# Kernel tuning notes

Measured on AMD Instinct MI355X. Metric: run time of the kernel, lower is better.

Reference implementation:

```python
import jax, jax.numpy as jnp
import numpy as np

EMB = 2048; H = 32; G = 8; D = 64; GS = H // G; EPS = 1e-6

def _rmsnorm(x, scale):
    x32 = x.astype(jnp.float32)
    var = jnp.mean(x32 * x32, axis=-1, keepdims=True)
    return (x32 * jax.lax.rsqrt(var + EPS) * scale).astype(x.dtype)

def _rope(x, cos, sin):
    # x: [B, h, S, D]; cos/sin: [S, D]
    d = x.shape[-1]
    x1, x2 = x[..., : d // 2], x[..., d // 2 :]
    rot = jnp.concatenate([-x2, x1], axis=-1)
    return (x * cos[None, None] + rot * sin[None, None]).astype(x.dtype)

def setup_inputs() -> dict:
    key = jax.random.key(0)
    ks = jax.random.split(key, 6)
    B, S = 2, 2048
    x = jax.random.normal(ks[0], (B, S, EMB), jnp.float32)
    # causal mask: True = blocked (masked_fill semantics)
    mask = jnp.triu(jnp.ones((S, S), dtype=bool), k=1)
    # standard RoPE tables, half-dim rotation, shape [S, D]
    inv_freq = 1.0 / (10000.0 ** (jnp.arange(0, D, 2, dtype=jnp.float32) / D))
    ang = jnp.arange(S, dtype=jnp.float32)[:, None] * inv_freq[None, :]  # [S, D/2]
    cos = jnp.concatenate([jnp.cos(ang), jnp.cos(ang)], axis=-1)
    sin = jnp.concatenate([jnp.sin(ang), jnp.sin(ang)], axis=-1)
    Wq = jax.random.normal(ks[1], (EMB, H * D), jnp.float32) * 0.02
    Wk = jax.random.normal(ks[2], (EMB, G * D), jnp.float32) * 0.02
    Wv = jax.random.normal(ks[3], (EMB, G * D), jnp.float32) * 0.02
    Wo = jax.random.normal(ks[4], (H * D, EMB), jnp.float32) * 0.02
    q_scale = jnp.ones((D,), jnp.float32)
    k_scale = jnp.ones((D,), jnp.float32)
    return {"x": x, "mask": mask, "cos": cos, "sin": sin, "Wq": Wq, "Wk": Wk,
            "Wv": Wv, "Wo": Wo, "q_scale": q_scale, "k_scale": k_scale}

def reference(x, mask, cos, sin, Wq, Wk, Wv, Wo, q_scale, k_scale):
    B, S, _ = x.shape
    q = (x @ Wq).reshape(B, S, H, D).transpose(0, 2, 1, 3)  # [B,H,S,D]
    k = (x @ Wk).reshape(B, S, G, D).transpose(0, 2, 1, 3)  # [B,G,S,D]
    v = (x @ Wv).reshape(B, S, G, D).transpose(0, 2, 1, 3)
    q = _rmsnorm(q, q_scale)
    k = _rmsnorm(k, k_scale)
    q = _rope(q, cos, sin)
    k = _rope(k, cos, sin)
    # GQA expansion (repeat_interleave over head dim)
    k = jnp.repeat(k, GS, axis=1)
    v = jnp.repeat(v, GS, axis=1)
    scale = 1.0 / np.float32(np.sqrt(D))
    s = jnp.einsum('bhqd,bhkd->bhqk', q.astype(jnp.float32), k.astype(jnp.float32)) * scale
    # flash path is causal regardless of `mask` arg; mask here equals causal
    s = jnp.where(mask[None, None], -jnp.inf, s)
    w = jax.nn.softmax(s, axis=-1)
    ctx = jnp.einsum('bhqk,bhkd->bhqd', w, v.astype(jnp.float32))
    ctx = ctx.transpose(0, 2, 1, 3).reshape(B, S, H * D)
    return ctx @ Wo
```

## Files before the change

### kernel.cpp

```cpp
#include <hip/hip_runtime.h>
#include <hip/hip_bf16.h>
#include <cstdint>
#include <cstddef>

#define EMB   2048
#define NH_   32
#define NG_   8
#define DH_   64
#define SEQ_  2048
#define BB_   2
#define MTOT  4096
#define LDQKV 3072

typedef __attribute__((ext_vector_type(8))) short s16x8;
typedef __attribute__((ext_vector_type(8))) unsigned short u16x8;
typedef __attribute__((ext_vector_type(4))) float f32x4;
typedef __attribute__((ext_vector_type(16))) float f32x16;
typedef __attribute__((ext_vector_type(4))) unsigned int u32x4;
typedef __attribute__((ext_vector_type(2))) unsigned int u32x2;
typedef __attribute__((ext_vector_type(2))) int i32x2;

__device__ __forceinline__ float bf2f(unsigned short u) {
  unsigned int x = (unsigned int)u << 16; return __uint_as_float(x);
}
__device__ __forceinline__ unsigned short f2bf(float f) {
  unsigned int x = __float_as_uint(f);
  x = x + 0x7FFFu + ((x >> 16) & 1u);
  return (unsigned short)(x >> 16);
}
__device__ __forceinline__ float ninf() { return __int_as_float(0xff800000); }
__device__ __forceinline__ unsigned int pack_bf2(float a, float b) {
  unsigned int r;
  asm("v_cvt_pk_bf16_f32 %0, %1, %2" : "=v"(r) : "v"(a), "v"(b));
  return r;
}
__device__ __forceinline__ void plswap(unsigned int& a, unsigned int& b) {
  i32x2 r = __builtin_amdgcn_permlane32_swap((int)a, (int)b, false, false);
  a = (unsigned int)r[0]; b = (unsigned int)r[1];
}
__device__ __forceinline__ void plswapf(float& a, float& b) {
  unsigned int ua = __float_as_uint(a), ub = __float_as_uint(b);
  plswap(ua, ub);
  a = __uint_as_float(ua); b = __uint_as_float(ub);
}

__device__ __forceinline__ void glds16(const void* g, void* l) {
  __builtin_amdgcn_global_load_lds((const __attribute__((address_space(1))) void*)g,
                                   (__attribute__((address_space(3))) void*)l, 16, 0, 0);
}

__global__ __launch_bounds__(256)
void cvtx(const float* __restrict__ x, unsigned short* __restrict__ xb) {
  size_t i = (size_t)blockIdx.x * 256 + threadIdx.x;
  float4 a = *(const float4*)(x + i * 8);
  float4 c = *(const float4*)(x + i * 8 + 4);
  u16x8 o;
  o[0] = f2bf(a.x); o[1] = f2bf(a.y); o[2] = f2bf(a.z); o[3] = f2bf(a.w);
  o[4] = f2bf(c.x); o[5] = f2bf(c.y); o[6] = f2bf(c.z); o[7] = f2bf(c.w);
  *(u16x8*)(xb + i * 8) = o;
}

__global__ __launch_bounds__(256)
void wtrans(const float* __restrict__ in, unsigned short* __restrict__ out, int N) {
  __shared__ float tile[64][65];
  const int tid = threadIdx.x;
  const int n0 = blockIdx.x * 64, k0 = blockIdx.y * 64;
  #pragma unroll
  for (int jj = 0; jj < 4; ++jj) {
    int r = (tid >> 4) + jj * 16;
    int c = (tid & 15) * 4;
    float4 v = *(const float4*)(in + (size_t)(k0 + r) * N + n0 + c);
    tile[r][c] = v.x; tile[r][c + 1] = v.y; tile[r][c + 2] = v.z; tile[r][c + 3] = v.w;
  }
  __syncthreads();
  #pragma unroll
  for (int rep = 0; rep < 2; ++rep) {
    int u = rep * 256 + tid;
    int nl = u >> 3, ch = u & 7;
    u16x8 o;
    #pragma unroll
    for (int e = 0; e < 8; ++e) o[e] = f2bf(tile[ch * 8 + e][nl]);
    *(u16x8*)(out + (size_t)(n0 + nl) * 2048 + k0 + ch * 8) = o;
  }
}

__global__ __launch_bounds__(512, 2)
void gemm256(const unsigned short* __restrict__ A, const unsigned short* __restrict__ Bt,
             unsigned short* __restrict__ C, int ldc) {
  __shared__ __align__(16) char L[4][32768];
  const int tid = threadIdx.x;
  const int wid = tid >> 6, lane = tid & 63;
  const int wm = wid >> 2, wn = wid & 3;
  const int grp = lane >> 4, l15 = lane & 15;
  const int bm = blockIdx.y * 256, bn = blockIdx.x * 256;
  const int nt = 2048 / 32;

  const int srow = tid >> 2;
  const int sc = (tid & 3) ^ (srow & 3);
  const int grp2 = grp ^ (l15 & 3);

  auto stage_ht = [&](int t, int h) {
    const unsigned short* src = (h < 2)
      ? A  + (size_t)(bm + h * 128 + srow) * 2048 + t * 32 + sc * 8
      : Bt + (size_t)(bn + (h - 2) * 128 + srow) * 2048 + t * 32 + sc * 8;
    glds16(src, &L[t & 3][h * 8192 + wid * 1024]);
  };

  f32x4 acc[8][4] = {};

  #pragma unroll
  for (int h = 0; h < 4; ++h) stage_ht(0, h);
  #pragma unroll
  for (int h = 0; h < 4; ++h) stage_ht(1, h);
  asm volatile("s_waitcnt vmcnt(4)" ::: "memory");
  __builtin_amdgcn_sched_barrier(0);
  __builtin_amdgcn_s_barrier();
  __builtin_amdgcn_sched_barrier(0);

  for (int t = 0; t < nt; ++t) {
    const char* Ab = &L[t & 3][0]     + (size_t)(wm * 128 + l15) * 64 + grp2 * 16;
    const char* Bb = &L[t & 3][16384] + (size_t)(wn * 64  + l15) * 64 + grp2 * 16;
    const bool pre = (t + 2 < nt);
    if (pre) { stage_ht(t + 2, 0); stage_ht(t + 2, 1); }
    s16x8 bf[4], af[4];
    #pragma unroll
    for (int j = 0; j < 4; ++j) bf[j] = *(const s16x8*)(Bb + j * 1024);
    #pragma unroll
    for (int i = 0; i < 4; ++i) af[i] = *(const s16x8*)(Ab + i * 1024);
    __builtin_amdgcn_s_setprio(1);
    #pragma unroll
    for (int i = 0; i < 4; ++i)
      #pragma unroll
      for (int j = 0; j < 4; ++j)
        acc[i][j] = __builtin_amdgcn_mfma_f32_16x16x32_bf16(af[i], bf[j], acc[i][j], 0, 0, 0);
    __builtin_amdgcn_s_setprio(0);
    if (pre) { stage_ht(t + 2, 2); stage_ht(t + 2, 3); }
    #pragma unroll
    for (int i = 0; i < 4; ++i) af[i] = *(const s16x8*)(Ab + (4 + i) * 1024);
    __builtin_amdgcn_s_setprio(1);
    #pragma unroll
    for (int i = 0; i < 4; ++i)
      #pragma unroll
      for (int j = 0; j < 4; ++j)
        acc[4 + i][j] = __builtin_amdgcn_mfma_f32_16x16x32_bf16(af[i], bf[j], acc[4 + i][j], 0, 0, 0);
    __builtin_amdgcn_s_setprio(0);
    if (t + 1 < nt) {
      if (pre) asm volatile("s_waitcnt vmcnt(4)" ::: "memory");
      else     asm volatile("s_waitcnt vmcnt(0)" ::: "memory");
      __builtin_amdgcn_sched_barrier(0);
      __builtin_amdgcn_s_barrier();
      __builtin_amdgcn_sched_barrier(0);
    }
  }

  #pragma unroll
  for (int i = 0; i < 8; ++i)
    #pragma unroll
    for (int j = 0; j < 4; ++j)
      #pragma unroll
      for (int r = 0; r < 4; ++r) {
        int row = bm + wm * 128 + i * 16 + grp * 4 + r;
        int col = bn + wn * 64 + j * 16 + l15;
        C[(size_t)row * ldc + col] = f2bf(acc[i][j][r]);
      }
}

template<int BF16OUT>
__global__ __launch_bounds__(256)
void gemm_bt(const unsigned short* __restrict__ A, const unsigned short* __restrict__ Bt,
             void* __restrict__ C, int ldc) {
  __shared__ __align__(16) unsigned short As[128 * 32];
  __shared__ __align__(16) unsigned short Bs[128 * 32];
  const int tid = threadIdx.x;
  const int w = tid >> 6, lane = tid & 63;
  const int grp = lane >> 4, l15 = lane & 15;
  const int wr = w >> 1, wc = w & 1;
  const int bm = blockIdx.y * 128, bn = blockIdx.x * 128;
  f32x4 acc[4][4] = {};
  for (int k0 = 0; k0 < 2048; k0 += 32) {
    #pragma unroll
    for (int j = 0; j < 2; ++j) {
      int unit = (j * 4 + w) * 64 + lane;
      int row = unit >> 2, ch = unit & 3;
      glds16(A  + (size_t)(bm + row) * 2048 + k0 + ch * 8, (char*)As + (j * 4 + w) * 1024);
      glds16(Bt + (size_t)(bn + row) * 2048 + k0 + ch * 8, (char*)Bs + (j * 4 + w) * 1024);
    }
    __syncthreads();
    s16x8 af[4], bf[4];
    #pragma unroll
    for (int i = 0; i < 4; ++i)
      af[i] = *(const s16x8*)((const char*)As + (wr * 64 + i * 16 + l15) * 64 + grp * 16);
    #pragma unroll
    for (int j = 0; j < 4; ++j)
      bf[j] = *(const s16x8*)((const char*)Bs + (wc * 64 + j * 16 + l15) * 64 + grp * 16);
    #pragma unroll
    for (int i = 0; i < 4; ++i)
      #pragma unroll
      for (int j = 0; j < 4; ++j)
        acc[i][j] = __builtin_amdgcn_mfma_f32_16x16x32_bf16(af[i], bf[j], acc[i][j], 0, 0, 0);
    __syncthreads();
  }
  #pragma unroll
  for (int i = 0; i < 4; ++i)
    #pragma unroll
    for (int j = 0; j < 4; ++j)
      #pragma unroll
      for (int r = 0; r < 4; ++r) {
        int row = bm + wr * 64 + i * 16 + grp * 4 + r;
        int col = bn + wc * 64 + j * 16 + l15;
        float v = acc[i][j][r];
        if (BF16OUT) ((unsigned short*)C)[(size_t)row * ldc + col] = f2bf(v);
        else         ((float*)C)[(size_t)row * ldc + col] = v;
      }
}

__global__ __launch_bounds__(256)
void rmsrope(unsigned short* __restrict__ t, const float* __restrict__ scale,
             const float* __restrict__ cs, const float* __restrict__ sn, int coff, float post) {
  int m = blockIdx.x * 4 + (threadIdx.x >> 6);
  int h = blockIdx.y;
  int lane = threadIdx.x & 63;
  int spos = m & (SEQ_ - 1);
  unsigned short* p = t + (size_t)m * LDQKV + coff + h * 64 + lane;
  float val = bf2f(*p);
  float sq = val * val;
  #pragma unroll
  for (int off = 32; off; off >>= 1) sq += __shfl_xor(sq, off);
  float r = rsqrtf(sq * (1.f / 64.f) + 1e-6f);
  float xn = val * r * scale[lane];
  float partner = __shfl_xor(xn, 32);
  float c = cs[spos * 64 + lane], s = sn[spos * 64 + lane];
  float o = (lane < 32) ? (xn * c - partner * s) : fmaf(xn, c, partner * s);
  *p = f2bf(o * post);
}

__global__ __launch_bounds__(256)
void kvtile(const unsigned short* __restrict__ qkv, unsigned short* __restrict__ Kt,
            unsigned short* __restrict__ Vt) {
  __shared__ unsigned short Kl[32][72];
  __shared__ unsigned short Vl[32][72];
  const int tid = threadIdx.x;
  const int kt = blockIdx.x;
  const int bg = blockIdx.y;
  const int b = bg >> 3, g = bg & 7;
  {
    int row = tid >> 3, ch = tid & 7;
    u16x8 kv = *(const u16x8*)(qkv + (size_t)(b * SEQ_ + kt * 32 + row) * LDQKV + 2048 + g * 64 + ch * 8);
    #pragma unroll
    for (int e = 0; e < 8; ++e) Kl[row][ch * 8 + e] = kv[e];
    u16x8 vv = *(const u16x8*)(qkv + (size_t)(b * SEQ_ + kt * 32 + row) * LDQKV + 2560 + g * 64 + ch * 8);
    #pragma unroll
    for (int e = 0; e < 8; ++e) Vl[row][ch * 8 + e] = vv[e];
  }
  __syncthreads();
  {
    int c = tid >> 5, row = tid & 31;
    u16x8 o;
    #pragma unroll
    for (int e = 0; e < 8; ++e) o[e] = Kl[row][c * 8 + e];
    *(u16x8*)(Kt + (((size_t)(bg * 64 + kt)) << 11) + (c * 32 + row) * 8) = o;
  }
  {
    int c = tid >> 6, d = tid & 63;
    u16x8 o;
    #pragma unroll
    for (int e = 0; e < 8; ++e) o[e] = Vl[c * 8 + e][d];
    *(u16x8*)(Vt + (((size_t)(bg * 64 + kt)) << 11) + (c * 64 + d) * 8) = o;
  }
}

__global__ __launch_bounds__(256)
void attn_mfma9(const unsigned short* __restrict__ qkv, const unsigned short* __restrict__ Ktg,
                const unsigned short* __restrict__ Vtg, unsigned short* __restrict__ ctx) {
  __shared__ __align__(16) unsigned short LA[8 * 1024];
  __shared__ __align__(16) unsigned short LB[8 * 1024];
  const int tid = threadIdx.x;
  const int w = tid >> 6, lane = tid & 63;
  const int l31 = lane & 31, half = lane >> 5;
  const int bid = blockIdx.x;
  const int x8 = bid & 7, r = bid >> 3;
  const int bg = x8 + 8 * (r & 1);
  const int rr = r >> 1;
  const int slot = rr >> 4, gi = rr & 15;
  const int qt = (slot == 0) ? (63 - gi) : (slot == 1) ? gi
               : (slot == 2) ? (47 - gi) : (16 + gi);
  const int b = bg >> 3, g = bg & 7, h = g * 4 + w;
  const int qbase = qt * 32;
  const int nkt = qt + 1;
  const int nit = (nkt + 1) >> 1;

  s16x8 qf[4];
  #pragma unroll
  for (int s = 0; s < 4; ++s)
    qf[s] = *(const s16x8*)(qkv + (size_t)(b * SEQ_ + qbase + l31) * LDQKV + h * 64 + half * 8 + s * 16);

  f32x16 acc0 = {}, acc1 = {};
  float l_st = 0.f;

  const size_t tbase = ((size_t)(bg * 64)) << 11;
  const int soff = (w << 9) + lane * 8;

  auto stage = [&](unsigned short* Lb, int pi) {
    const int kt0 = 2 * pi, kt1 = 2 * pi + 1;
    glds16(Ktg + tbase + ((size_t)kt0 << 11) + soff, (char*)Lb + (w << 10));
    glds16(Vtg + tbase + ((size_t)kt0 << 11) + soff, (char*)Lb + 8192 + (w << 10));
    if (kt1 < nkt) {
      glds16(Ktg + tbase + ((size_t)kt1 << 11) + soff, (char*)Lb + 4096 + (w << 10));
      glds16(Vtg + tbase + ((size_t)kt1 << 11) + soff, (char*)Lb + 12288 + (w << 10));
    }
  };

  auto sub = [&](const char* Kb, const char* Vb, bool diag, float& lsum) {
    s16x8 KF0 = *(const s16x8*)(Kb + (((0 + half) << 5) + l31) * 16);
    s16x8 KF1 = *(const s16x8*)(Kb + (((2 + half) << 5) + l31) * 16);
    s16x8 KF2 = *(const s16x8*)(Kb + (((4 + half) << 5) + l31) * 16);
    s16x8 KF3 = *(const s16x8*)(Kb + (((6 + half) << 5) + l31) * 16);
    s16x8 vf00 = *(const s16x8*)(Vb + (((half) << 6) + l31) * 16);
    s16x8 vf01 = *(const s16x8*)(Vb + (((2 + half) << 6) + l31) * 16);
    s16x8 vf10 = *(const s16x8*)(Vb + (((half) << 6) + 32 + l31) * 16);
    s16x8 vf11 = *(const s16x8*)(Vb + (((2 + half) << 6) + 32 + l31) * 16);
    f32x16 st = {};
    __builtin_amdgcn_s_setprio(1);
    st = __builtin_amdgcn_mfma_f32_32x32x16_bf16(KF0, qf[0], st, 0, 0, 0);
    st = __builtin_amdgcn_mfma_f32_32x32x16_bf16(KF1, qf[1], st, 0, 0, 0);
    st = __builtin_amdgcn_mfma_f32_32x32x16_bf16(KF2, qf[2], st, 0, 0, 0);
    st = __builtin_amdgcn_mfma_f32_32x32x16_bf16(KF3, qf[3], st, 0, 0, 0);
    __builtin_amdgcn_s_setprio(0);
    if (diag) {
      #pragma unroll
      for (int r2 = 0; r2 < 16; ++r2) {
        int key = (r2 & 3) + 8 * (r2 >> 2) + 4 * half;
        if (key > l31) st[r2] = ninf();
      }
    }
    float p[16];
    #pragma unroll
    for (int r2 = 0; r2 < 16; ++r2) p[r2] = exp2f(st[r2]);
    float s8[8];
    #pragma unroll
    for (int r2 = 0; r2 < 8; ++r2) s8[r2] = p[r2] + p[r2 + 8];
    lsum += ((s8[0] + s8[1]) + (s8[2] + s8[3])) + ((s8[4] + s8[5]) + (s8[6] + s8[7]));
    unsigned int PK[8];
    #pragma unroll
    for (int j = 0; j < 8; ++j) PK[j] = pack_bf2(p[2 * j], p[2 * j + 1]);
    plswap(PK[0], PK[2]); plswap(PK[1], PK[3]);
    plswap(PK[4], PK[6]); plswap(PK[5], PK[7]);
    u32x4 pb0u, pb1u;
    pb0u[0] = PK[0]; pb0u[1] = PK[1]; pb0u[2] = PK[2]; pb0u[3] = PK[3];
    pb1u[0] = PK[4]; pb1u[1] = PK[5]; pb1u[2] = PK[6]; pb1u[3] = PK[7];
    s16x8 pb0 = __builtin_bit_cast(s16x8, pb0u);
    s16x8 pb1 = __builtin_bit_cast(s16x8, pb1u);
    __builtin_amdgcn_s_setprio(1);
    acc0 = __builtin_amdgcn_mfma_f32_32x32x16_bf16(vf00, pb0, acc0, 0, 0, 0);
    acc1 = __builtin_amdgcn_mfma_f32_32x32x16_bf16(vf10, pb0, acc1, 0, 0, 0);
    acc0 = __builtin_amdgcn_mfma_f32_32x32x16_bf16(vf01, pb1, acc0, 0, 0, 0);
    acc1 = __builtin_amdgcn_mfma_f32_32x32x16_bf16(vf11, pb1, acc1, 0, 0, 0);
    __builtin_amdgcn_s_setprio(0);
  };

  auto pair_body = [&](const unsigned short* Lb, int pi) {
    const int kt0 = 2 * pi, kt1 = 2 * pi + 1;
    float lsum = 0.f;
    sub((const char*)Lb, (const char*)Lb + 8192, kt0 == qt, lsum);
    if (kt1 < nkt)
      sub((const char*)Lb + 4096, (const char*)Lb + 12288, kt1 == qt, lsum);
    { float a2 = lsum, b2 = lsum; plswapf(a2, b2); lsum = a2 + b2; }
    l_st += lsum;
  };

  stage(LA, 0);
  int pi = 0;
  while (true) {
    __syncthreads();
    if (pi + 1 < nit) stage(LB, pi + 1);
    pair_body(LA, pi);
    ++pi; if (pi >= nit) break;
    __syncthreads();
    if (pi + 1 < nit) stage(LA, pi + 1);
    pair_body(LB, pi);
    ++pi; if (pi >= nit) break;
  }

  const float linv = 1.f / l_st;
  unsigned short* orow = ctx + (size_t)(b * SEQ_ + qbase + l31) * 2048 + h * 64;
  #pragma unroll
  for (int dt = 0; dt < 2; ++dt) {
    #pragma unroll
    for (int rq = 0; rq < 4; ++rq) {
      const int rr2 = rq * 4;
      const int d0 = dt * 32 + 8 * rq + 4 * half;
      float a0 = (dt ? acc1[rr2]     : acc0[rr2])     * linv;
      float a1 = (dt ? acc1[rr2 + 1] : acc0[rr2 + 1]) * linv;
      float a2 = (dt ? acc1[rr2 + 2] : acc0[rr2 + 2]) * linv;
      float a3 = (dt ? acc1[rr2 + 3] : acc0[rr2 + 3]) * linv;
      u32x2 o;
      o[0] = pack_bf2(a0, a1);
      o[1] = pack_bf2(a2, a3);
      *(u32x2*)(orow + d0) = o;
    }
  }
}

extern "C" void kernel_launch(void* const* d_in, const int* in_sizes, int n_in,
                              void* d_out, int out_size, void* d_ws, size_t ws_size,
                              hipStream_t stream) {
  const float* x  = (const float*)d_in[0];
  const float* cs = (const float*)d_in[2];
  const float* sn = (const float*)d_in[3];
  const float* Wq = (const float*)d_in[4];
  const float* Wk = (const float*)d_in[5];
  const float* Wv = (const float*)d_in[6];
  const float* Wo = (const float*)d_in[7];
  const float* qs = (const float*)d_in[8];
  const float* ks = (const float*)d_in[9];
  float* out = (float*)d_out;

  unsigned short* xb  = (unsigned short*)d_ws;
  unsigned short* Wt  = xb  + (size_t)4096 * 2048;
  unsigned short* Wot = Wt  + (size_t)3072 * 2048;
  unsigned short* qkv = Wot + (size_t)2048 * 2048;
  unsigned short* vTb = qkv + (size_t)4096 * 3072;
  unsigned short* ctx = vTb + (size_t)16 * 64 * 2048;
  unsigned short* Ktt = xb;

  cvtx<<<4096, 256, 0, stream>>>(x, xb);
  wtrans<<<dim3(32, 32), 256, 0, stream>>>(Wq, Wt, 2048);
  wtrans<<<dim3(8, 32),  256, 0, stream>>>(Wk, Wt + (size_t)2048 * 2048, 512);
  wtrans<<<dim3(8, 32),  256, 0, stream>>>(Wv, Wt + (size_t)2560 * 2048, 512);
  wtrans<<<dim3(32, 32), 256, 0, stream>>>(Wo, Wot, 2048);
  gemm256<<<dim3(12, 16), 512, 0, stream>>>(xb, Wt, qkv, 3072);
  rmsrope<<<dim3(1024, 32), 256, 0, stream>>>(qkv, qs, cs, sn, 0, 0.18033688f);
  rmsrope<<<dim3(1024, 8),  256, 0, stream>>>(qkv, ks, cs, sn, 2048, 1.0f);
  kvtile<<<dim3(64, 16), 256, 0, stream>>>(qkv, Ktt, vTb);
  attn_mfma9<<<1024, 256, 0, stream>>>(qkv, Ktt, vTb, ctx);
  gemm_bt<0><<<dim3(16, 32), 256, 0, stream>>>(ctx, Wot, out, 2048);
}
```

Before: 220.5 us.

## Fuse prep kernels, fold RMSNorm+RoPE into consumers, reuse pipelined GEMM for output

Merges the x conversion and four weight transposes into one prep launch. Removes the standalone rmsrope passes by applying the K norm and RoPE inside kvtile and the Q norm, RoPE and softmax scale inside the attention kernel's Q load. The output projection now uses the templated pipelined 256-row GEMM with a 128-wide N tile and fp32 output, replacing the simpler gemm_bt. The aim is fewer launches and no extra read-modify-write pass over the qkv buffer. The cost is more register pressure in attention, and launch bounds drop to one block per SIMD.

```diff
diff --git a/kernel.cpp b/kernel.cpp
--- a/kernel.cpp
+++ b/kernel.cpp
@@ -11,6 +11,7 @@
 #define BB_   2
 #define MTOT  4096
 #define LDQKV 3072
+#define SM_C  0.18033688f
 
 typedef __attribute__((ext_vector_type(8))) short s16x8;
 typedef __attribute__((ext_vector_type(8))) unsigned short u16x8;
@@ -50,21 +51,30 @@
 }
 
 __global__ __launch_bounds__(256)
-void cvtx(const float* __restrict__ x, unsigned short* __restrict__ xb) {
-  size_t i = (size_t)blockIdx.x * 256 + threadIdx.x;
-  float4 a = *(const float4*)(x + i * 8);
-  float4 c = *(const float4*)(x + i * 8 + 4);
-  u16x8 o;
-  o[0] = f2bf(a.x); o[1] = f2bf(a.y); o[2] = f2bf(a.z); o[3] = f2bf(a.w);
-  o[4] = f2bf(c.x); o[5] = f2bf(c.y); o[6] = f2bf(c.z); o[7] = f2bf(c.w);
-  *(u16x8*)(xb + i * 8) = o;
-}
-
-__global__ __launch_bounds__(256)
-void wtrans(const float* __restrict__ in, unsigned short* __restrict__ out, int N) {
+void prep(const float* __restrict__ x, const float* __restrict__ Wq,
+          const float* __restrict__ Wk, const float* __restrict__ Wv,
+          const float* __restrict__ Wo, unsigned short* __restrict__ xb,
+          unsigned short* __restrict__ Wt, unsigned short* __restrict__ Wot) {
   __shared__ float tile[64][65];
   const int tid = threadIdx.x;
-  const int n0 = blockIdx.x * 64, k0 = blockIdx.y * 64;
+  const int bid = blockIdx.x;
+  if (bid < 4096) {
+    size_t i = (size_t)bid * 256 + tid;
+    float4 a = *(const float4*)(x + i * 8);
+    float4 c = *(const float4*)(x + i * 8 + 4);
+    u16x8 o;
+    o[0] = f2bf(a.x); o[1] = f2bf(a.y); o[2] = f2bf(a.z); o[3] = f2bf(a.w);
+    o[4] = f2bf(c.x); o[5] = f2bf(c.y); o[6] = f2bf(c.z); o[7] = f2bf(c.w);
+    *(u16x8*)(xb + i * 8) = o;
+    return;
+  }
+  const float* in; unsigned short* out; int N; int local;
+  if (bid < 5120)      { in = Wq; out = Wt;                       N = 2048; local = bid - 4096; }
+  else if (bid < 5376) { in = Wk; out = Wt + (size_t)2048 * 2048; N = 512;  local = bid - 5120; }
+  else if (bid < 5632) { in = Wv; out = Wt + (size_t)2560 * 2048; N = 512;  local = bid - 5376; }
+  else                 { in = Wo; out = Wot;                      N = 2048; local = bid - 5632; }
+  const int ntile = N >> 6;
+  const int n0 = (local % ntile) * 64, k0 = (local / ntile) * 64;
   #pragma unroll
   for (int jj = 0; jj < 4; ++jj) {
     int r = (tid >> 4) + jj * 16;
@@ -84,16 +94,21 @@
   }
 }
 
-__global__ __launch_bounds__(512, 2)
+template<int BN, int F32OUT>
+__global__ __launch_bounds__(512, 1)
 void gemm256(const unsigned short* __restrict__ A, const unsigned short* __restrict__ Bt,
-             unsigned short* __restrict__ C, int ldc) {
-  __shared__ __align__(16) char L[4][32768];
+             void* __restrict__ C, int ldc) {
+  constexpr int NST = 2 + BN / 128;
+  constexpr int BUF = 16384 + BN * 64;
+  constexpr int WN = BN / 64;
+  constexpr int RW = 256 / (8 / WN);
+  __shared__ __align__(16) char L[4][BUF];
   const int tid = threadIdx.x;
   const int wid = tid >> 6, lane = tid & 63;
-  const int wm = wid >> 2, wn = wid & 3;
+  const int wm = wid / WN, wn = wid % WN;
   const int grp = lane >> 4, l15 = lane & 15;
-  const int bm = blockIdx.y * 256, bn = blockIdx.x * 256;
-  const int nt = 2048 / 32;
+  const int bm = blockIdx.y * 256, bn = blockIdx.x * BN;
+  const int nt = 64;
 
   const int srow = tid >> 2;
   const int sc = (tid & 3) ^ (srow & 3);
@@ -106,20 +121,21 @@
     glds16(src, &L[t & 3][h * 8192 + wid * 1024]);
   };
 
-  f32x4 acc[8][4] = {};
-
-  #pragma unroll
-  for (int h = 0; h < 4; ++h) stage_ht(0, h);
-  #pragma unroll
-  for (int h = 0; h < 4; ++h) stage_ht(1, h);
-  asm volatile("s_waitcnt vmcnt(4)" ::: "memory");
+  f32x4 acc[RW / 16][4] = {};
+
+  #pragma unroll
+  for (int h = 0; h < NST; ++h) stage_ht(0, h);
+  #pragma unroll
+  for (int h = 0; h < NST; ++h) stage_ht(1, h);
+  if constexpr (BN == 256) asm volatile("s_waitcnt vmcnt(4)" ::: "memory");
+  else                     asm volatile("s_waitcnt vmcnt(3)" ::: "memory");
   __builtin_amdgcn_sched_barrier(0);
   __builtin_amdgcn_s_barrier();
   __builtin_amdgcn_sched_barrier(0);
 
   for (int t = 0; t < nt; ++t) {
-    const char* Ab = &L[t & 3][0]     + (size_t)(wm * 128 + l15) * 64 + grp2 * 16;
-    const char* Bb = &L[t & 3][16384] + (size_t)(wn * 64  + l15) * 64 + grp2 * 16;
+    const char* Ab = &L[t & 3][0]     + (size_t)(wm * RW + l15) * 64 + grp2 * 16;
+    const char* Bb = &L[t & 3][16384] + (size_t)(wn * 64 + l15) * 64 + grp2 * 16;
     const bool pre = (t + 2 < nt);
     if (pre) { stage_ht(t + 2, 0); stage_ht(t + 2, 1); }
     s16x8 bf[4], af[4];
@@ -134,19 +150,27 @@
       for (int j = 0; j < 4; ++j)
         acc[i][j] = __builtin_amdgcn_mfma_f32_16x16x32_bf16(af[i], bf[j], acc[i][j], 0, 0, 0);
     __builtin_amdgcn_s_setprio(0);
-    if (pre) { stage_ht(t + 2, 2); stage_ht(t + 2, 3); }
-    #pragma unroll
-    for (int i = 0; i < 4; ++i) af[i] = *(const s16x8*)(Ab + (4 + i) * 1024);
-    __builtin_amdgcn_s_setprio(1);
-    #pragma unroll
-    for (int i = 0; i < 4; ++i)
-      #pragma unroll
-      for (int j = 0; j < 4; ++j)
-        acc[4 + i][j] = __builtin_amdgcn_mfma_f32_16x16x32_bf16(af[i], bf[j], acc[4 + i][j], 0, 0, 0);
-    __builtin_amdgcn_s_setprio(0);
+    if constexpr (BN == 256) {
+      if (pre) { stage_ht(t + 2, 2); stage_ht(t + 2, 3); }
+      #pragma unroll
+      for (int i = 0; i < 4; ++i) af[i] = *(const s16x8*)(Ab + (4 + i) * 1024);
+      __builtin_amdgcn_s_setprio(1);
+      #pragma unroll
+      for (int i = 0; i < 4; ++i)
+        #pragma unroll
+        for (int j = 0; j < 4; ++j)
+          acc[4 + i][j] = __builtin_amdgcn_mfma_f32_16x16x32_bf16(af[i], bf[j], acc[4 + i][j], 0, 0, 0);
+      __builtin_amdgcn_s_setprio(0);
+    } else {
+      if (pre) stage_ht(t + 2, 2);
+    }
     if (t + 1 < nt) {
-      if (pre) asm volatile("s_waitcnt vmcnt(4)" ::: "memory");
-      else     asm volatile("s_waitcnt vmcnt(0)" ::: "memory");
+      if (pre) {
+        if constexpr (BN == 256) asm volatile("s_waitcnt vmcnt(4)" ::: "memory");
+        else                     asm volatile("s_waitcnt vmcnt(3)" ::: "memory");
+      } else {
+        asm volatile("s_waitcnt vmcnt(0)" ::: "memory");
+      }
       __builtin_amdgcn_sched_barrier(0);
       __builtin_amdgcn_s_barrier();
       __builtin_amdgcn_sched_barrier(0);
@@ -154,89 +178,23 @@
   }
 
   #pragma unroll
-  for (int i = 0; i < 8; ++i)
+  for (int i = 0; i < RW / 16; ++i)
     #pragma unroll
     for (int j = 0; j < 4; ++j)
       #pragma unroll
       for (int r = 0; r < 4; ++r) {
-        int row = bm + wm * 128 + i * 16 + grp * 4 + r;
+        int row = bm + wm * RW + i * 16 + grp * 4 + r;
         int col = bn + wn * 64 + j * 16 + l15;
-        C[(size_t)row * ldc + col] = f2bf(acc[i][j][r]);
+        float v = acc[i][j][r];
+        if (F32OUT) ((float*)C)[(size_t)row * ldc + col] = v;
+        else        ((unsigned short*)C)[(size_t)row * ldc + col] = f2bf(v);
       }
 }
 
-template<int BF16OUT>
 __global__ __launch_bounds__(256)
-void gemm_bt(const unsigned short* __restrict__ A, const unsigned short* __restrict__ Bt,
-             void* __restrict__ C, int ldc) {
-  __shared__ __align__(16) unsigned short As[128 * 32];
-  __shared__ __align__(16) unsigned short Bs[128 * 32];
-  const int tid = threadIdx.x;
-  const int w = tid >> 6, lane = tid & 63;
-  const int grp = lane >> 4, l15 = lane & 15;
-  const int wr = w >> 1, wc = w & 1;
-  const int bm = blockIdx.y * 128, bn = blockIdx.x * 128;
-  f32x4 acc[4][4] = {};
-  for (int k0 = 0; k0 < 2048; k0 += 32) {
-    #pragma unroll
-    for (int j = 0; j < 2; ++j) {
-      int unit = (j * 4 + w) * 64 + lane;
-      int row = unit >> 2, ch = unit & 3;
-      glds16(A  + (size_t)(bm + row) * 2048 + k0 + ch * 8, (char*)As + (j * 4 + w) * 1024);
-      glds16(Bt + (size_t)(bn + row) * 2048 + k0 + ch * 8, (char*)Bs + (j * 4 + w) * 1024);
-    }
-    __syncthreads();
-    s16x8 af[4], bf[4];
-    #pragma unroll
-    for (int i = 0; i < 4; ++i)
-      af[i] = *(const s16x8*)((const char*)As + (wr * 64 + i * 16 + l15) * 64 + grp * 16);
-    #pragma unroll
-    for (int j = 0; j < 4; ++j)
-      bf[j] = *(const s16x8*)((const char*)Bs + (wc * 64 + j * 16 + l15) * 64 + grp * 16);
-    #pragma unroll
-    for (int i = 0; i < 4; ++i)
-      #pragma unroll
-      for (int j = 0; j < 4; ++j)
-        acc[i][j] = __builtin_amdgcn_mfma_f32_16x16x32_bf16(af[i], bf[j], acc[i][j], 0, 0, 0);
-    __syncthreads();
-  }
-  #pragma unroll
-  for (int i = 0; i < 4; ++i)
-    #pragma unroll
-    for (int j = 0; j < 4; ++j)
-      #pragma unroll
-      for (int r = 0; r < 4; ++r) {
-        int row = bm + wr * 64 + i * 16 + grp * 4 + r;
-        int col = bn + wc * 64 + j * 16 + l15;
-        float v = acc[i][j][r];
-        if (BF16OUT) ((unsigned short*)C)[(size_t)row * ldc + col] = f2bf(v);
-        else         ((float*)C)[(size_t)row * ldc + col] = v;
-      }
-}
-
-__global__ __launch_bounds__(256)
-void rmsrope(unsigned short* __restrict__ t, const float* __restrict__ scale,
-             const float* __restrict__ cs, const float* __restrict__ sn, int coff, float post) {
-  int m = blockIdx.x * 4 + (threadIdx.x >> 6);
-  int h = blockIdx.y;
-  int lane = threadIdx.x & 63;
-  int spos = m & (SEQ_ - 1);
-  unsigned short* p = t + (size_t)m * LDQKV + coff + h * 64 + lane;
-  float val = bf2f(*p);
-  float sq = val * val;
-  #pragma unroll
-  for (int off = 32; off; off >>= 1) sq += __shfl_xor(sq, off);
-  float r = rsqrtf(sq * (1.f / 64.f) + 1e-6f);
-  float xn = val * r * scale[lane];
-  float partner = __shfl_xor(xn, 32);
-  float c = cs[spos * 64 + lane], s = sn[spos * 64 + lane];
-  float o = (lane < 32) ? (xn * c - partner * s) : fmaf(xn, c, partner * s);
-  *p = f2bf(o * post);
-}
-
-__global__ __launch_bounds__(256)
-void kvtile(const unsigned short* __restrict__ qkv, unsigned short* __restrict__ Kt,
-            unsigned short* __restrict__ Vt) {
+void kvtile_rms(const unsigned short* __restrict__ qkv, const float* __restrict__ ksc,
+                const float* __restrict__ cs, const float* __restrict__ sn,
+                unsigned short* __restrict__ Kt, unsigned short* __restrict__ Vt) {
   __shared__ unsigned short Kl[32][72];
   __shared__ unsigned short Vl[32][72];
   const int tid = threadIdx.x;
@@ -244,11 +202,29 @@
   const int bg = blockIdx.y;
   const int b = bg >> 3, g = bg & 7;
   {
-    int row = tid >> 3, ch = tid & 7;
-    u16x8 kv = *(const u16x8*)(qkv + (size_t)(b * SEQ_ + kt * 32 + row) * LDQKV + 2048 + g * 64 + ch * 8);
-    #pragma unroll
-    for (int e = 0; e < 8; ++e) Kl[row][ch * 8 + e] = kv[e];
-    u16x8 vv = *(const u16x8*)(qkv + (size_t)(b * SEQ_ + kt * 32 + row) * LDQKV + 2560 + g * 64 + ch * 8);
+    const int row = tid >> 3, ch = tid & 7;
+    const int spos = kt * 32 + row;
+    u16x8 kv = *(const u16x8*)(qkv + (size_t)(b * SEQ_ + spos) * LDQKV + 2048 + g * 64 + ch * 8);
+    float v[8]; float sq = 0.f;
+    #pragma unroll
+    for (int e = 0; e < 8; ++e) { v[e] = bf2f(kv[e]); sq += v[e] * v[e]; }
+    sq += __shfl_xor(sq, 1); sq += __shfl_xor(sq, 2); sq += __shfl_xor(sq, 4);
+    const float rn = rsqrtf(sq * (1.f / 64.f) + 1e-6f);
+    float xn[8];
+    #pragma unroll
+    for (int e = 0; e < 8; ++e) xn[e] = v[e] * rn * ksc[ch * 8 + e];
+    float pn[8];
+    #pragma unroll
+    for (int e = 0; e < 8; ++e) pn[e] = __shfl_xor(xn[e], 4);
+    const bool lo = (ch < 4);
+    #pragma unroll
+    for (int e = 0; e < 8; ++e) {
+      int d = ch * 8 + e;
+      float c = cs[spos * 64 + d], si = sn[spos * 64 + d];
+      float o = lo ? (xn[e] * c - pn[e] * si) : fmaf(xn[e], c, pn[e] * si);
+      Kl[row][d] = f2bf(o);
+    }
+    u16x8 vv = *(const u16x8*)(qkv + (size_t)(b * SEQ_ + spos) * LDQKV + 2560 + g * 64 + ch * 8);
     #pragma unroll
     for (int e = 0; e < 8; ++e) Vl[row][ch * 8 + e] = vv[e];
   }
@@ -270,8 +246,10 @@
 }
 
 __global__ __launch_bounds__(256)
-void attn_mfma9(const unsigned short* __restrict__ qkv, const unsigned short* __restrict__ Ktg,
-                const unsigned short* __restrict__ Vtg, unsigned short* __restrict__ ctx) {
+void attn_mfma10(const unsigned short* __restrict__ qkv, const float* __restrict__ qsc,
+                 const float* __restrict__ cs, const float* __restrict__ sn,
+                 const unsigned short* __restrict__ Ktg, const unsigned short* __restrict__ Vtg,
+                 unsigned short* __restrict__ ctx) {
   __shared__ __align__(16) unsigned short LA[8 * 1024];
   __shared__ __align__(16) unsigned short LB[8 * 1024];
   const int tid = threadIdx.x;
@@ -290,9 +268,41 @@
   const int nit = (nkt + 1) >> 1;
 
   s16x8 qf[4];
-  #pragma unroll
-  for (int s = 0; s < 4; ++s)
-    qf[s] = *(const s16x8*)(qkv + (size_t)(b * SEQ_ + qbase + l31) * LDQKV + h * 64 + half * 8 + s * 16);
+  {
+    const int spos = qbase + l31;
+    float qv[4][8]; float sq = 0.f;
+    #pragma unroll
+    for (int s = 0; s < 4; ++s) {
+      u16x8 raw = *(const u16x8*)(qkv + (size_t)(b * SEQ_ + spos) * LDQKV + h * 64 + half * 8 + s * 16);
+      #pragma unroll
+      for (int e = 0; e < 8; ++e) { qv[s][e] = bf2f(raw[e]); sq += qv[s][e] * qv[s][e]; }
+    }
+    sq += __shfl_xor(sq, 32);
+    const float rn = rsqrtf(sq * (1.f / 64.f) + 1e-6f);
+    float xn[4][8];
+    #pragma unroll
+    for (int s = 0; s < 4; ++s)
+      #pragma unroll
+      for (int e = 0; e < 8; ++e) xn[s][e] = qv[s][e] * rn * qsc[s * 16 + half * 8 + e];
+    float qo[4][8];
+    #pragma unroll
+    for (int s = 0; s < 2; ++s)
+      #pragma unroll
+      for (int e = 0; e < 8; ++e) {
+        int d = s * 16 + half * 8 + e;
+        float c0 = cs[spos * 64 + d],      s0 = sn[spos * 64 + d];
+        float c1 = cs[spos * 64 + d + 32], s1 = sn[spos * 64 + d + 32];
+        qo[s][e]     = (xn[s][e] * c0 - xn[s + 2][e] * s0) * SM_C;
+        qo[s + 2][e] = fmaf(xn[s + 2][e], c1, xn[s][e] * s1) * SM_C;
+      }
+    #pragma unroll
+    for (int s = 0; s < 4; ++s) {
+      u32x4 t;
+      t[0] = pack_bf2(qo[s][0], qo[s][1]); t[1] = pack_bf2(qo[s][2], qo[s][3]);
+      t[2] = pack_bf2(qo[s][4], qo[s][5]); t[3] = pack_bf2(qo[s][6], qo[s][7]);
+      qf[s] = __builtin_bit_cast(s16x8, t);
+    }
+  }
 
   f32x16 acc0 = {}, acc1 = {};
   float l_st = 0.f;
@@ -423,15 +433,9 @@
   unsigned short* ctx = vTb + (size_t)16 * 64 * 2048;
   unsigned short* Ktt = xb;
 
-  cvtx<<<4096, 256, 0, stream>>>(x, xb);
-  wtrans<<<dim3(32, 32), 256, 0, stream>>>(Wq, Wt, 2048);
-  wtrans<<<dim3(8, 32),  256, 0, stream>>>(Wk, Wt + (size_t)2048 * 2048, 512);
-  wtrans<<<dim3(8, 32),  256, 0, stream>>>(Wv, Wt + (size_t)2560 * 2048, 512);
-  wtrans<<<dim3(32, 32), 256, 0, stream>>>(Wo, Wot, 2048);
-  gemm256<<<dim3(12, 16), 512, 0, stream>>>(xb, Wt, qkv, 3072);
-  rmsrope<<<dim3(1024, 32), 256, 0, stream>>>(qkv, qs, cs, sn, 0, 0.18033688f);
-  rmsrope<<<dim3(1024, 8),  256, 0, stream>>>(qkv, ks, cs, sn, 2048, 1.0f);
-  kvtile<<<dim3(64, 16), 256, 0, stream>>>(qkv, Ktt, vTb);
-  attn_mfma9<<<1024, 256, 0, stream>>>(qkv, Ktt, vTb, ctx);
-  gemm_bt<0><<<dim3(16, 32), 256, 0, stream>>>(ctx, Wot, out, 2048);
-}
+  prep<<<6656, 256, 0, stream>>>(x, Wq, Wk, Wv, Wo, xb, Wt, Wot);
+  gemm256<256, 0><<<dim3(12, 16), 512, 0, stream>>>(xb, Wt, qkv, 3072);
+  kvtile_rms<<<dim3(64, 16), 256, 0, stream>>>(qkv, ks, cs, sn, Ktt, vTb);
+  attn_mfma10<<<1024, 256, 0, stream>>>(qkv, qs, cs, sn, Ktt, vTb, ctx);
+  gemm256<128, 1><<<dim3(16, 16), 512, 0, stream>>>(ctx, Wot, out, 2048);
+}
```

After: 193.0 us. -12.5%, faster.
